# Kernel optimization log

Hardware: AMD Instinct MI355X
Metric: run time of the kernel (lower is better)

## Reference

```python
import jax, jax.numpy as jnp
import numpy as np

BETA = 0.25
N_E = 1024
E_DIM = 256


def setup_inputs() -> dict:
    key = jax.random.key(0)
    k1, k2 = jax.random.split(key)
    z = jax.random.normal(k1, (32, E_DIM, 2048), dtype=jnp.float32)
    # embedding initialized uniform(-1/n_e, 1/n_e) in the original
    codebook = jax.random.uniform(k2, (N_E, E_DIM), dtype=jnp.float32,
                                  minval=-1.0 / N_E, maxval=1.0 / N_E)
    return {"z": z, "codebook": codebook}


def reference(z, codebook):
    sg = jax.lax.stop_gradient
    # z: (B, C, T) -> (B, T, C)
    zt = jnp.transpose(z, (0, 2, 1))
    B, T, C = zt.shape
    zf = zt.reshape(-1, C)  # (N, C)
    # squared euclidean distances to codebook: (N, n_e)
    d = (jnp.sum(zf * zf, axis=1, keepdims=True)
         + jnp.sum(codebook * codebook, axis=1)
         - 2.0 * jnp.einsum('nc,kc->nk', zf, codebook))
    min_encoding_indices = jnp.argmin(d, axis=1)  # (N,)
    # one-hot encodings (the original scatters into a dense (N, n_e) matrix)
    min_encodings = jax.nn.one_hot(min_encoding_indices, codebook.shape[0],
                                   dtype=z.dtype)
    # gather == one_hot @ codebook, same math, efficient form
    z_q = codebook[min_encoding_indices].reshape(B, T, C)
    loss = (jnp.mean((sg(z_q) - zt) ** 2)
            + BETA * jnp.mean((z_q - sg(zt)) ** 2))
    # straight-through estimator
    z_q_st = zt + sg(z_q - zt)
    e_mean = jnp.mean(min_encodings, axis=0)
    perplexity = jnp.exp(-jnp.sum(e_mean * jnp.log(e_mean + 1e-10)))
    z_q_out = jnp.transpose(z_q_st, (0, 2, 1))  # back to (B, C, T)
    return (loss, z_q_out, perplexity, min_encodings,
            min_encoding_indices[:, None])
```

## Files before the change

kernel.cpp:

```cpp
#include <hip/hip_runtime.h>

#define BB    32
#define CDIM  256
#define TT    2048
#define NE    1024
#define NROWS (BB * TT)
#define NELEM (BB * CDIM * TT)

#define BM   128
#define NCH  8

#define FBW 2.5e-4f

typedef unsigned short u16;
typedef unsigned int   u32;
typedef __attribute__((ext_vector_type(8))) short s16x8;
typedef __attribute__((ext_vector_type(4))) float f32x4;

__device__ __forceinline__ u16 f2bf(float f) {
  u32 u = __float_as_uint(f);
  u += 0x7fffu + ((u >> 16) & 1u);
  return (u16)(u >> 16);
}

__device__ __forceinline__ float np_sq_sum128(const float* p, int stride) {
#pragma clang fp contract(off)
  float r[8];
#pragma unroll
  for (int j = 0; j < 8; j++) {
    float v = p[(size_t)j * stride];
    r[j] = v * v;
  }
  for (int i = 8; i < 128; i += 8) {
#pragma unroll
    for (int j = 0; j < 8; j++) {
      float v = p[(size_t)(i + j) * stride];
      float s = v * v;
      r[j] += s;
    }
  }
  return ((r[0] + r[1]) + (r[2] + r[3])) + ((r[4] + r[5]) + (r[6] + r[7]));
}

__global__ __launch_bounds__(256) void e2_kernel(const float* __restrict__ cb,
                                                 float* __restrict__ e2) {
#pragma clang fp contract(off)
  int k = blockIdx.x * 256 + threadIdx.x;
  if (k >= NE) return;
  const float* p = cb + (size_t)k * CDIM;
  float h0 = np_sq_sum128(p, 1);
  float h1 = np_sq_sum128(p + 128, 1);
  e2[k] = h0 + h1;
}

__global__ __launch_bounds__(256) void z2_kernel(const float* __restrict__ z,
                                                 float* __restrict__ z2) {
#pragma clang fp contract(off)
  int n = blockIdx.x * 256 + threadIdx.x;
  if (n >= NROWS) return;
  int b = n >> 11;
  int t = n & (TT - 1);
  const float* p = z + (size_t)b * CDIM * TT + t;
  float h0 = np_sq_sum128(p, TT);
  float h1 = np_sq_sum128(p + (size_t)128 * TT, TT);
  z2[n] = h0 + h1;
}

__global__ __launch_bounds__(256) void transpose_cb_kernel(
    const float* __restrict__ cb, float* __restrict__ cbT) {
  __shared__ float tile[32][33];
  int tx = threadIdx.x & 31, ty = threadIdx.x >> 5;
  int n0 = blockIdx.x * 32, c0 = blockIdx.y * 32;
#pragma unroll
  for (int i = 0; i < 4; i++)
    tile[ty + 8 * i][tx] = cb[(size_t)(n0 + ty + 8 * i) * CDIM + c0 + tx];
  __syncthreads();
#pragma unroll
  for (int i = 0; i < 4; i++)
    cbT[(size_t)(c0 + ty + 8 * i) * NE + n0 + tx] = tile[tx][ty + 8 * i];
}

__global__ __launch_bounds__(256) void convert_cb_kernel(
    const float* __restrict__ cb, u16* __restrict__ cbhi,
    u16* __restrict__ cblo) {
  int i = blockIdx.x * 256 + threadIdx.x;
  float v  = cb[i];
  u16  h   = f2bf(v);
  float hf = __uint_as_float((u32)h << 16);
  cbhi[i] = h;
  cblo[i] = f2bf(v - hf);
}

__global__ __launch_bounds__(256) void convert_z_kernel(
    const float* __restrict__ z, u16* __restrict__ zhi,
    u16* __restrict__ zlo) {
  __shared__ float tile[32][33];
  int bx = blockIdx.x;
  int b  = bx >> 9;
  int r  = bx & 511;
  int c0 = (r >> 6) << 5;
  int t0 = (r & 63) << 5;
  int tx = threadIdx.x & 31, ty = threadIdx.x >> 5;
#pragma unroll
  for (int i = 0; i < 4; i++) {
    int c = c0 + ty + 8 * i;
    tile[ty + 8 * i][tx] = z[((size_t)b * CDIM + c) * TT + t0 + tx];
  }
  __syncthreads();
#pragma unroll
  for (int i = 0; i < 4; i++) {
    int tl = ty + 8 * i;
    size_t n = (size_t)b * TT + t0 + tl;
    float v  = tile[tx][tl];
    u16  h   = f2bf(v);
    float hf = __uint_as_float((u32)h << 16);
    zhi[n * CDIM + c0 + tx] = h;
    zlo[n * CDIM + c0 + tx] = f2bf(v - hf);
  }
}

struct StageMem {
  u16 ah[2][128][32];
  u16 al[2][128][32];
  u16 bh[2][128][32];
  u16 bl[2][128][32];
};
struct RedMem {
  float rv1[BM][2];
  float rv2[BM][2];
  int   ri1[BM][2];
};

#define GLL(g, l)                                                            \
  __builtin_amdgcn_global_load_lds(                                          \
      (const __attribute__((address_space(1))) void*)(g),                    \
      (__attribute__((address_space(3))) void*)(l), 16, 0, 0)

__global__ __launch_bounds__(256, 2) void dist_argmin_kernel(
    const u16* __restrict__ zhi, const u16* __restrict__ zlo,
    const u16* __restrict__ cbhi, const u16* __restrict__ cblo,
    const float* __restrict__ e2, int* __restrict__ out_idx,
    int* __restrict__ fb_cnt, int* __restrict__ fb_list) {
  __shared__ union SMem {
    StageMem st;
    RedMem   rd;
  } sm;

  const int tid  = threadIdx.x;
  const int lane = tid & 63;
  const int wid  = tid >> 6;
  const int wr   = wid >> 1;
  const int wc   = wid & 1;
  const int lr   = lane & 15;
  const int kg   = lane >> 4;
  const int row0 = blockIdx.x * BM;
  const int sw   = (lr >> 1) & 3;

  const u16* zhiB = zhi + (size_t)row0 * CDIM;
  const u16* zloB = zlo + (size_t)row0 * CDIM;

  float bv1[16], bv2[16];
  int   bi1[16];
#pragma unroll
  for (int i = 0; i < 16; i++) {
    bv1[i] = __builtin_inff(); bv2[i] = __builtin_inff(); bi1[i] = 0;
  }

  for (int ch = 0; ch < NCH; ch++) {
    const int code0 = ch * 128;
    const u16* bhB = cbhi + (size_t)code0 * CDIM;
    const u16* blB = cblo + (size_t)code0 * CDIM;

    f32x4 acc[4][4];
#pragma unroll
    for (int a = 0; a < 4; a++)
#pragma unroll
      for (int b = 0; b < 4; b++) acc[a][b] = (f32x4){0.f, 0.f, 0.f, 0.f};

    for (int ph = 0; ph < 4; ph++) {
      const int kc = ph * 64;
      __syncthreads();
#pragma unroll
      for (int rr = 0; rr < 4; rr++) {
        int s   = tid + rr * 256;
        int sub = s >> 9;
        int s9  = s & 511;
        int row = s9 >> 2, pos = s9 & 3;
        int q   = pos ^ ((row >> 1) & 3);
        size_t ko = (size_t)(kc + sub * 32 + q * 8);
        GLL(zhiB + (size_t)row * CDIM + ko, &sm.st.ah[sub][row][pos * 8]);
        GLL(zloB + (size_t)row * CDIM + ko, &sm.st.al[sub][row][pos * 8]);
        GLL(bhB  + (size_t)row * CDIM + ko, &sm.st.bh[sub][row][pos * 8]);
        GLL(blB  + (size_t)row * CDIM + ko, &sm.st.bl[sub][row][pos * 8]);
      }
      __syncthreads();

      const int pos = kg ^ sw;
#pragma unroll
      for (int sub = 0; sub < 2; sub++) {
        s16x8 zah[4], zal[4], ebh[4], ebl[4];
#pragma unroll
        for (int t = 0; t < 4; t++) {
          zah[t] = *(const s16x8*)&sm.st.ah[sub][wr * 64 + t * 16 + lr][pos * 8];
          zal[t] = *(const s16x8*)&sm.st.al[sub][wr * 64 + t * 16 + lr][pos * 8];
          ebh[t] = *(const s16x8*)&sm.st.bh[sub][wc * 64 + t * 16 + lr][pos * 8];
          ebl[t] = *(const s16x8*)&sm.st.bl[sub][wc * 64 + t * 16 + lr][pos * 8];
        }
#pragma unroll
        for (int tr = 0; tr < 4; tr++)
#pragma unroll
          for (int tc = 0; tc < 4; tc++) {
            acc[tr][tc] = __builtin_amdgcn_mfma_f32_16x16x32_bf16(
                zah[tr], ebh[tc], acc[tr][tc], 0, 0, 0);
            acc[tr][tc] = __builtin_amdgcn_mfma_f32_16x16x32_bf16(
                zah[tr], ebl[tc], acc[tr][tc], 0, 0, 0);
            acc[tr][tc] = __builtin_amdgcn_mfma_f32_16x16x32_bf16(
                zal[tr], ebh[tc], acc[tr][tc], 0, 0, 0);
          }
      }
    }

    float e2c[4];
#pragma unroll
    for (int tc = 0; tc < 4; tc++)
      e2c[tc] = e2[code0 + wc * 64 + tc * 16 + lr];
#pragma unroll
    for (int tr = 0; tr < 4; tr++)
#pragma unroll
      for (int rg = 0; rg < 4; rg++) {
        const int rs = tr * 4 + rg;
#pragma unroll
        for (int tc = 0; tc < 4; tc++) {
          float a = acc[tr][tc][rg];
          float d = e2c[tc] - 2.0f * a;
          int code = code0 + wc * 64 + tc * 16 + lr;
          if (d < bv2[rs]) {
            if (d < bv1[rs]) { bv2[rs] = bv1[rs]; bv1[rs] = d; bi1[rs] = code; }
            else bv2[rs] = d;
          }
        }
      }
  }

#pragma unroll
  for (int rs = 0; rs < 16; rs++) {
#pragma unroll
    for (int m = 1; m <= 8; m <<= 1) {
      float o1 = __shfl_xor(bv1[rs], m);
      float o2 = __shfl_xor(bv2[rs], m);
      int   oi = __shfl_xor(bi1[rs], m);
      float mx = fmaxf(bv1[rs], o1);
      if (o1 < bv1[rs]) { bv1[rs] = o1; bi1[rs] = oi; }
      bv2[rs] = fminf(fminf(bv2[rs], o2), mx);
    }
  }

  __syncthreads();
  if (lr == 0) {
#pragma unroll
    for (int tr = 0; tr < 4; tr++)
#pragma unroll
      for (int rg = 0; rg < 4; rg++) {
        int rs = tr * 4 + rg;
        int r  = wr * 64 + tr * 16 + kg * 4 + rg;
        sm.rd.rv1[r][wc] = bv1[rs];
        sm.rd.rv2[r][wc] = bv2[rs];
        sm.rd.ri1[r][wc] = bi1[rs];
      }
  }
  __syncthreads();
  if (tid < BM) {
    float a1 = sm.rd.rv1[tid][0], b1 = sm.rd.rv1[tid][1];
    float a2 = sm.rd.rv2[tid][0], b2 = sm.rd.rv2[tid][1];
    int   ai = sm.rd.ri1[tid][0], bi = sm.rd.ri1[tid][1];
    float v1 = fminf(a1, b1);
    int   i1 = (b1 < a1) ? bi : ai;
    float v2 = fminf(fminf(a2, b2), fmaxf(a1, b1));
    int n = row0 + tid;
    out_idx[n] = i1;
    if (v2 - v1 <= FBW) {
      int slot = atomicAdd(fb_cnt, 1);
      fb_list[slot] = n;
    }
  }
}

__global__ __launch_bounds__(256) void fallback_kernel(
    const float* __restrict__ z, const float* __restrict__ cbT,
    const float* __restrict__ z2, const float* __restrict__ e2,
    const int* __restrict__ fb_cnt, const int* __restrict__ fb_list,
    int* __restrict__ out_idx) {
#pragma clang fp contract(off)
  __shared__ float zrow[CDIM];
  __shared__ float rv[4];
  __shared__ int   ri[4];
  const int cnt  = *fb_cnt;
  const int tid  = threadIdx.x;
  const int lane = tid & 63;
  const int w    = tid >> 6;
  for (int q = blockIdx.x; q < cnt; q += gridDim.x) {
    const int n = fb_list[q];
    const int b = n >> 11, t = n & (TT - 1);
    __syncthreads();
    zrow[tid] = z[((size_t)b * CDIM + tid) * TT + t];
    __syncthreads();
    const float z2n = z2[n];
    const int   c0  = w * 256 + lane;
    const float* ct = cbT + c0;
    float acc0 = 0.f, acc1 = 0.f, acc2 = 0.f, acc3 = 0.f;
    for (int k = 0; k < CDIM; k++) {
      float zk = zrow[k];
      const float* p = ct + (size_t)k * NE;
      acc0 = acc0 + zk * p[0];
      acc1 = acc1 + zk * p[64];
      acc2 = acc2 + zk * p[128];
      acc3 = acc3 + zk * p[192];
    }
    float bv = __builtin_inff(); int bi = 0;
    float dd;
    dd = (z2n + e2[c0 +   0]) - 2.0f * acc0; if (dd < bv) { bv = dd; bi = c0; }
    dd = (z2n + e2[c0 +  64]) - 2.0f * acc1; if (dd < bv) { bv = dd; bi = c0 + 64; }
    dd = (z2n + e2[c0 + 128]) - 2.0f * acc2; if (dd < bv) { bv = dd; bi = c0 + 128; }
    dd = (z2n + e2[c0 + 192]) - 2.0f * acc3; if (dd < bv) { bv = dd; bi = c0 + 192; }
#pragma unroll
    for (int m = 1; m < 64; m <<= 1) {
      float ov = __shfl_xor(bv, m);
      int   oi = __shfl_xor(bi, m);
      if (ov < bv || (ov == bv && oi < bi)) { bv = ov; bi = oi; }
    }
    if (lane == 0) { rv[w] = bv; ri[w] = bi; }
    __syncthreads();
    if (tid == 0) {
      float v = rv[0]; int i = ri[0];
#pragma unroll
      for (int x = 1; x < 4; x++)
        if (rv[x] < v || (rv[x] == v && ri[x] < i)) { v = rv[x]; i = ri[x]; }
      out_idx[n] = i;
    }
  }
}

__global__ __launch_bounds__(256) void zq_loss_kernel(
    const float* __restrict__ z, const float* __restrict__ cb,
    const int* __restrict__ idx, float* __restrict__ zq_out,
    double* __restrict__ loss_acc) {
#pragma clang fp contract(off)
  __shared__ double sh[256];
  double local = 0.0;
  int stride = gridDim.x * blockDim.x;
  for (int i = blockIdx.x * blockDim.x + threadIdx.x; i < NELEM; i += stride) {
    int t = i & (TT - 1);
    int b = i >> 19;
    int c = (i >> 11) & (CDIM - 1);
    int n = (b << 11) | t;
    float zq   = cb[(size_t)idx[n] * CDIM + c];
    float zv   = z[i];
    float diff = zq - zv;
    zq_out[i]  = zv + diff;
    float sq   = diff * diff;
    local += (double)sq;
  }
  sh[threadIdx.x] = local;
  __syncthreads();
  for (int s = 128; s > 0; s >>= 1) {
    if (threadIdx.x < s) sh[threadIdx.x] += sh[threadIdx.x + s];
    __syncthreads();
  }
  if (threadIdx.x == 0) atomicAdd(loss_acc, sh[0]);
}

__global__ __launch_bounds__(256) void onehot_kernel(
    const int* __restrict__ idx, float* __restrict__ oh,
    float* __restrict__ idx_out, int* __restrict__ cnt) {
  int row  = blockIdx.x * 4 + (threadIdx.x >> 6);
  int lane = threadIdx.x & 63;
  int k    = idx[row];
  if (lane == 0) {
    idx_out[row] = (float)k;
    atomicAdd(&cnt[k], 1);
  }
  float4* dst = (float4*)(oh + (size_t)row * NE);
#pragma unroll
  for (int i = 0; i < 4; i++) {
    int c4   = i * 64 + lane;
    int base = c4 * 4;
    float4 v = {0.f, 0.f, 0.f, 0.f};
    if (k >= base && k < base + 4) ((float*)&v)[k - base] = 1.0f;
    dst[c4] = v;
  }
}

__global__ __launch_bounds__(1024) void finalize_kernel(
    const int* __restrict__ cnt, const double* __restrict__ loss_acc,
    float* __restrict__ out_loss, float* __restrict__ out_perp) {
#pragma clang fp contract(off)
  __shared__ float sh[1024];
  int t = threadIdx.x;
  float em = (float)cnt[t] / 65536.0f;
  sh[t] = em * logf(em + 1e-10f);
  __syncthreads();
  for (int s = 512; s > 0; s >>= 1) {
    if (t < s) sh[t] += sh[t + s];
    __syncthreads();
  }
  if (t == 0) {
    *out_perp = expf(-sh[0]);
    double m  = *loss_acc / (double)NELEM;
    float mf  = (float)m;
    float bt  = 0.25f * mf;
    *out_loss = mf + bt;
  }
}

extern "C" void kernel_launch(void* const* d_in, const int* in_sizes, int n_in,
                              void* d_out, int out_size, void* d_ws,
                              size_t ws_size, hipStream_t stream) {
  const float* z  = (const float*)d_in[0];
  const float* cb = (const float*)d_in[1];
  float* out = (float*)d_out;

  int*    ws_idx   = (int*)d_ws;
  int*    ws_cnt   = ws_idx + NROWS;
  int*    ws_fbcnt = ws_cnt + NE;
  int*    ws_pad   = ws_fbcnt + 1;
  double* ws_loss  = (double*)(ws_pad + 1);
  float*  ws_e2    = (float*)(ws_loss + 1);
  float*  ws_z2    = ws_e2 + NE;
  int*    ws_fbl   = (int*)(ws_z2 + NROWS);
  float*  ws_cbT   = (float*)(ws_fbl + NROWS);

  float* out_loss = out;
  float* out_zq   = out + 1;
  float* out_perp = out + 1 + (size_t)NELEM;
  float* out_oh   = out + 2 + (size_t)NELEM;
  float* out_idx  = out + 2 + (size_t)NELEM + (size_t)NROWS * NE;

  uintptr_t sc = ((uintptr_t)out_oh + 63) & ~(uintptr_t)63;
  u16*   zhi  = (u16*)sc;
  u16*   zlo  = zhi + (size_t)NROWS * CDIM;
  u16*   cbhi = zlo + (size_t)NROWS * CDIM;
  u16*   cblo = cbhi + (size_t)NE * CDIM;

  hipMemsetAsync(ws_cnt, 0, NE * sizeof(int) + 2 * sizeof(int) + sizeof(double),
                 stream);

  transpose_cb_kernel<<<dim3(NE / 32, CDIM / 32), 256, 0, stream>>>(cb, ws_cbT);
  convert_cb_kernel<<<NE * CDIM / 256, 256, 0, stream>>>(cb, cbhi, cblo);
  convert_z_kernel<<<BB * 512, 256, 0, stream>>>(z, zhi, zlo);
  e2_kernel<<<NE / 256, 256, 0, stream>>>(cb, ws_e2);
  z2_kernel<<<NROWS / 256, 256, 0, stream>>>(z, ws_z2);
  dist_argmin_kernel<<<NROWS / BM, 256, 0, stream>>>(
      zhi, zlo, cbhi, cblo, ws_e2, ws_idx, ws_fbcnt, ws_fbl);
  fallback_kernel<<<2048, 256, 0, stream>>>(z, ws_cbT, ws_z2, ws_e2, ws_fbcnt,
                                            ws_fbl, ws_idx);
  zq_loss_kernel<<<2048, 256, 0, stream>>>(z, cb, ws_idx, out_zq, ws_loss);
  onehot_kernel<<<NROWS / 4, 256, 0, stream>>>(ws_idx, out_oh, out_idx,
                                               ws_cnt);
  finalize_kernel<<<1, 1024, 0, stream>>>(ws_cnt, ws_loss, out_loss, out_perp);
}
```

Before: 923.8 us.

## Double-buffer LDS staging across a flattened k-plane loop to overlap loads with MFMA

Flattens the code-chunk and k-phase loops into a single 64-plane loop. Each plane is 32 wide in k and is staged into one of two LDS buffers with global_load_lds, so the next plane's loads are issued before the MFMAs on the current plane run. This replaces the two __syncthreads per phase with a single barrier per plane plus an explicit vmcnt wait. The distance epilogue and accumulator reset now run every 8 planes. The intent is to hide global-load latency behind compute, at the cost of finer-grained barriers and hand-placed scheduling fences.

```diff
diff --git a/kernel.cpp b/kernel.cpp
--- a/kernel.cpp
+++ b/kernel.cpp
@@ -8,7 +8,7 @@
 #define NELEM (BB * CDIM * TT)
 
 #define BM   128
-#define NCH  8
+#define NPL  64
 
 #define FBW 2.5e-4f
 
@@ -120,8 +120,8 @@
 }
 
 struct StageMem {
-  u16 ah[2][128][32];
-  u16 al[2][128][32];
+  u16 ah[2][BM][32];
+  u16 al[2][BM][32];
   u16 bh[2][128][32];
   u16 bl[2][128][32];
 };
@@ -159,6 +159,29 @@
   const u16* zhiB = zhi + (size_t)row0 * CDIM;
   const u16* zloB = zlo + (size_t)row0 * CDIM;
 
+  const int s0 = tid,        s1 = tid + 256;
+  const int r0 = s0 >> 2,    r1 = s1 >> 2;
+  const int p0 = s0 & 3,     p1 = s1 & 3;
+  const int q0 = p0 ^ ((r0 >> 1) & 3);
+  const int q1 = p1 ^ ((r1 >> 1) & 3);
+
+#define STAGE_PLANE(pl, buf)                                                 \
+  do {                                                                       \
+    const int ch_   = (pl) >> 3;                                             \
+    const int kc_   = ((pl) & 7) * 32;                                       \
+    const int c0_   = ch_ * 128;                                             \
+    const size_t k0_ = (size_t)(kc_ + q0 * 8);                               \
+    const size_t k1_ = (size_t)(kc_ + q1 * 8);                               \
+    GLL(zhiB + (size_t)r0 * CDIM + k0_, &sm.st.ah[buf][r0][p0 * 8]);         \
+    GLL(zhiB + (size_t)r1 * CDIM + k1_, &sm.st.ah[buf][r1][p1 * 8]);         \
+    GLL(zloB + (size_t)r0 * CDIM + k0_, &sm.st.al[buf][r0][p0 * 8]);         \
+    GLL(zloB + (size_t)r1 * CDIM + k1_, &sm.st.al[buf][r1][p1 * 8]);         \
+    GLL(cbhi + (size_t)(c0_ + r0) * CDIM + k0_, &sm.st.bh[buf][r0][p0 * 8]); \
+    GLL(cbhi + (size_t)(c0_ + r1) * CDIM + k1_, &sm.st.bh[buf][r1][p1 * 8]); \
+    GLL(cblo + (size_t)(c0_ + r0) * CDIM + k0_, &sm.st.bl[buf][r0][p0 * 8]); \
+    GLL(cblo + (size_t)(c0_ + r1) * CDIM + k1_, &sm.st.bl[buf][r1][p1 * 8]); \
+  } while (0)
+
   float bv1[16], bv2[16];
   int   bi1[16];
 #pragma unroll
@@ -166,81 +189,78 @@
     bv1[i] = __builtin_inff(); bv2[i] = __builtin_inff(); bi1[i] = 0;
   }
 
-  for (int ch = 0; ch < NCH; ch++) {
-    const int code0 = ch * 128;
-    const u16* bhB = cbhi + (size_t)code0 * CDIM;
-    const u16* blB = cblo + (size_t)code0 * CDIM;
-
-    f32x4 acc[4][4];
-#pragma unroll
-    for (int a = 0; a < 4; a++)
-#pragma unroll
-      for (int b = 0; b < 4; b++) acc[a][b] = (f32x4){0.f, 0.f, 0.f, 0.f};
-
-    for (int ph = 0; ph < 4; ph++) {
-      const int kc = ph * 64;
-      __syncthreads();
-#pragma unroll
-      for (int rr = 0; rr < 4; rr++) {
-        int s   = tid + rr * 256;
-        int sub = s >> 9;
-        int s9  = s & 511;
-        int row = s9 >> 2, pos = s9 & 3;
-        int q   = pos ^ ((row >> 1) & 3);
-        size_t ko = (size_t)(kc + sub * 32 + q * 8);
-        GLL(zhiB + (size_t)row * CDIM + ko, &sm.st.ah[sub][row][pos * 8]);
-        GLL(zloB + (size_t)row * CDIM + ko, &sm.st.al[sub][row][pos * 8]);
-        GLL(bhB  + (size_t)row * CDIM + ko, &sm.st.bh[sub][row][pos * 8]);
-        GLL(blB  + (size_t)row * CDIM + ko, &sm.st.bl[sub][row][pos * 8]);
+  f32x4 acc[4][4];
+#pragma unroll
+  for (int a = 0; a < 4; a++)
+#pragma unroll
+    for (int b = 0; b < 4; b++) acc[a][b] = (f32x4){0.f, 0.f, 0.f, 0.f};
+
+  int cur = 0;
+  STAGE_PLANE(0, 0);
+  asm volatile("s_waitcnt vmcnt(0)" ::: "memory");
+  __builtin_amdgcn_sched_barrier(0);
+
+  const int pos = kg ^ sw;
+
+  for (int t = 0; t < NPL; ++t) {
+    __builtin_amdgcn_s_barrier();
+    __builtin_amdgcn_sched_barrier(0);
+
+    if (t < NPL - 1) STAGE_PLANE(t + 1, cur ^ 1);
+
+    s16x8 zah[4], zal[4], ebh[4], ebl[4];
+#pragma unroll
+    for (int t4 = 0; t4 < 4; t4++) {
+      zah[t4] = *(const s16x8*)&sm.st.ah[cur][wr * 64 + t4 * 16 + lr][pos * 8];
+      zal[t4] = *(const s16x8*)&sm.st.al[cur][wr * 64 + t4 * 16 + lr][pos * 8];
+      ebh[t4] = *(const s16x8*)&sm.st.bh[cur][wc * 64 + t4 * 16 + lr][pos * 8];
+      ebl[t4] = *(const s16x8*)&sm.st.bl[cur][wc * 64 + t4 * 16 + lr][pos * 8];
+    }
+#pragma unroll
+    for (int tr = 0; tr < 4; tr++)
+#pragma unroll
+      for (int tc = 0; tc < 4; tc++) {
+        acc[tr][tc] = __builtin_amdgcn_mfma_f32_16x16x32_bf16(
+            zah[tr], ebh[tc], acc[tr][tc], 0, 0, 0);
+        acc[tr][tc] = __builtin_amdgcn_mfma_f32_16x16x32_bf16(
+            zah[tr], ebl[tc], acc[tr][tc], 0, 0, 0);
+        acc[tr][tc] = __builtin_amdgcn_mfma_f32_16x16x32_bf16(
+            zal[tr], ebh[tc], acc[tr][tc], 0, 0, 0);
       }
-      __syncthreads();
-
-      const int pos = kg ^ sw;
-#pragma unroll
-      for (int sub = 0; sub < 2; sub++) {
-        s16x8 zah[4], zal[4], ebh[4], ebl[4];
-#pragma unroll
-        for (int t = 0; t < 4; t++) {
-          zah[t] = *(const s16x8*)&sm.st.ah[sub][wr * 64 + t * 16 + lr][pos * 8];
-          zal[t] = *(const s16x8*)&sm.st.al[sub][wr * 64 + t * 16 + lr][pos * 8];
-          ebh[t] = *(const s16x8*)&sm.st.bh[sub][wc * 64 + t * 16 + lr][pos * 8];
-          ebl[t] = *(const s16x8*)&sm.st.bl[sub][wc * 64 + t * 16 + lr][pos * 8];
-        }
-#pragma unroll
-        for (int tr = 0; tr < 4; tr++)
+
+    if ((t & 7) == 7) {
+      const int code0 = (t >> 3) * 128;
+      float e2c[4];
+#pragma unroll
+      for (int tc = 0; tc < 4; tc++)
+        e2c[tc] = e2[code0 + wc * 64 + tc * 16 + lr];
+#pragma unroll
+      for (int tr = 0; tr < 4; tr++)
+#pragma unroll
+        for (int rg = 0; rg < 4; rg++) {
+          const int rs = tr * 4 + rg;
 #pragma unroll
           for (int tc = 0; tc < 4; tc++) {
-            acc[tr][tc] = __builtin_amdgcn_mfma_f32_16x16x32_bf16(
-                zah[tr], ebh[tc], acc[tr][tc], 0, 0, 0);
-            acc[tr][tc] = __builtin_amdgcn_mfma_f32_16x16x32_bf16(
-                zah[tr], ebl[tc], acc[tr][tc], 0, 0, 0);
-            acc[tr][tc] = __builtin_amdgcn_mfma_f32_16x16x32_bf16(
-                zal[tr], ebh[tc], acc[tr][tc], 0, 0, 0);
-          }
-      }
-    }
-
-    float e2c[4];
-#pragma unroll
-    for (int tc = 0; tc < 4; tc++)
-      e2c[tc] = e2[code0 + wc * 64 + tc * 16 + lr];
-#pragma unroll
-    for (int tr = 0; tr < 4; tr++)
-#pragma unroll
-      for (int rg = 0; rg < 4; rg++) {
-        const int rs = tr * 4 + rg;
-#pragma unroll
-        for (int tc = 0; tc < 4; tc++) {
-          float a = acc[tr][tc][rg];
-          float d = e2c[tc] - 2.0f * a;
-          int code = code0 + wc * 64 + tc * 16 + lr;
-          if (d < bv2[rs]) {
-            if (d < bv1[rs]) { bv2[rs] = bv1[rs]; bv1[rs] = d; bi1[rs] = code; }
-            else bv2[rs] = d;
+            float a = acc[tr][tc][rg];
+            float d = e2c[tc] - 2.0f * a;
+            int code = code0 + wc * 64 + tc * 16 + lr;
+            if (d < bv2[rs]) {
+              if (d < bv1[rs]) { bv2[rs] = bv1[rs]; bv1[rs] = d; bi1[rs] = code; }
+              else bv2[rs] = d;
+            }
           }
         }
-      }
-  }
+#pragma unroll
+      for (int a = 0; a < 4; a++)
+#pragma unroll
+        for (int b = 0; b < 4; b++) acc[a][b] = (f32x4){0.f, 0.f, 0.f, 0.f};
+    }
+
+    asm volatile("s_waitcnt vmcnt(0)" ::: "memory");
+    __builtin_amdgcn_sched_barrier(0);
+    cur ^= 1;
+  }
+#undef STAGE_PLANE
 
 #pragma unroll
   for (int rs = 0; rs < 16; rs++) {
```

Result: faster. 816.2 us (-11.7%).
